# Kernel optimization log

Measured on AMD Instinct MI355X. Metric: run time of the kernel, lower is better.

## Reference

```python
import jax, jax.numpy as jnp
import numpy as np

N, D_IN, D_HID, D_OUT, E = 8192, 1024, 4096, 1024, 8
N_ACTIVE = max(1, int(E * 0.625))  # 5
TEMP = float(np.e)               # temperature = np.e in source


def setup_inputs() -> dict:
    key = jax.random.key(0)
    ks = jax.random.split(key, 4)
    return {
        "x": jax.random.normal(ks[0], (N, D_IN), jnp.float32),
        "gate_w": jax.random.normal(ks[1], (D_IN, E), jnp.float32) * 0.02,
        "gate_b": jnp.zeros((E,), jnp.float32),
        "w1": jax.random.normal(ks[2], (E, D_IN, D_HID), jnp.float32) * 0.02,
        "b1": jnp.zeros((E, D_HID), jnp.float32),
        "w2": jax.random.normal(ks[3], (E, D_HID, D_OUT), jnp.float32) * 0.02,
        "b2": jnp.zeros((E, D_OUT), jnp.float32),
    }


def reference(x, gate_w, gate_b, w1, b1, w2, b2):
    # Gate: softmax over experts at temperature e, then top-k mask + renormalize
    scores = (x @ gate_w + gate_b) / TEMP                 # [N, E]
    probs = jax.nn.softmax(scores, axis=-1)               # [N, E]
    _, topk_idx = jax.lax.top_k(probs, N_ACTIVE)          # [N, k]
    mask = jax.nn.one_hot(topk_idx, E, dtype=probs.dtype).sum(axis=-2)  # [N, E]
    weights = probs * mask
    weights = weights / (weights.sum(axis=-1, keepdims=True) + 1e-8)
    # Dense all-experts FFN (dropout is eval-mode identity)
    h = jax.nn.relu(jnp.einsum('nd,edh->neh', x, w1) + b1)   # [N, E, d_hid]
    e_out = jnp.einsum('neh,eho->neo', h, w2) + b2           # [N, E, d_out]
    # Camp A (first E/2 experts) added, camp G subtracted: out = out_a - out_g
    sign = jnp.where(jnp.arange(E) < E // 2, 1.0, -1.0)      # [E]
    return jnp.einsum('ne,neo->no', weights * sign, e_out)   # [N, d_out]
```

## Files before the change

kernel.cpp:

```cpp
#include <hip/hip_runtime.h>
#include <hip/hip_bf16.h>
#include <cmath>


typedef _Float16 f16;
typedef _Float16 f16x8 __attribute__((ext_vector_type(8)));
typedef _Float16 f16x4 __attribute__((ext_vector_type(4)));
typedef float f32x4 __attribute__((ext_vector_type(4)));

#define NROWS 8192
#define DIN   1024
#define DHID  4096
#define DOUT  1024
#define NEXP  8

#define OFF_SGATE 0u
#define OFF_XH    262144u
#define OFF_W1T   17039360u
#define OFF_W2T   84148224u
#define OFF_HHS   151257088u
#define OFF_PART  688128000u
#define NEED_PRIMARY 755236864ull
#define NEED_FALLBACK 218365952ull

__device__ __forceinline__ void gload_lds16(const void* gsrc, void* ldsdst) {
  __builtin_amdgcn_global_load_lds(
      (const __attribute__((address_space(1))) unsigned int*)gsrc,
      (__attribute__((address_space(3))) unsigned int*)ldsdst, 16, 0, 0);
}

__global__ void gate_kernel(const float* __restrict__ x,
                            const float* __restrict__ gw,
                            const float* __restrict__ gb,
                            float* __restrict__ sgate) {
  const int row = blockIdx.x * 4 + (threadIdx.x >> 6);
  const int l = threadIdx.x & 63;
  const float* xr = x + (size_t)row * DIN;
  float acc[8] = {0.f,0.f,0.f,0.f,0.f,0.f,0.f,0.f};
#pragma unroll
  for (int j = 0; j < 16; ++j) {
    const int k = l + 64 * j;
    const float xv = xr[k];
    const float4 g0 = *(const float4*)(gw + (size_t)k * 8);
    const float4 g1 = *(const float4*)(gw + (size_t)k * 8 + 4);
    acc[0] += xv * g0.x; acc[1] += xv * g0.y; acc[2] += xv * g0.z; acc[3] += xv * g0.w;
    acc[4] += xv * g1.x; acc[5] += xv * g1.y; acc[6] += xv * g1.z; acc[7] += xv * g1.w;
  }
#pragma unroll
  for (int off = 32; off > 0; off >>= 1) {
#pragma unroll
    for (int e = 0; e < 8; ++e) acc[e] += __shfl_xor(acc[e], off, 64);
  }
  if (l == 0) {
    const float invT = 0.36787944117144233f;
    float p[8]; float mx = -1e30f;
#pragma unroll
    for (int e = 0; e < 8; ++e) { p[e] = (acc[e] + gb[e]) * invT; mx = fmaxf(mx, p[e]); }
    float S = 0.f;
#pragma unroll
    for (int e = 0; e < 8; ++e) { p[e] = expf(p[e] - mx); S += p[e]; }
    const float inv = 1.0f / S;
#pragma unroll
    for (int e = 0; e < 8; ++e) p[e] *= inv;
    bool keep[8] = {true,true,true,true,true,true,true,true};
    for (int t = 0; t < 3; ++t) {
      float pmin = 1e30f; int mi = -1;
      for (int e = 0; e < 8; ++e)
        if (keep[e] && (p[e] < pmin || (p[e] == pmin && e > mi))) { pmin = p[e]; mi = e; }
      keep[mi] = false;
    }
    float wsum = 0.f;
#pragma unroll
    for (int e = 0; e < 8; ++e) if (keep[e]) wsum += p[e];
    const float rinv = 1.0f / (wsum + 1e-8f);
#pragma unroll
    for (int e = 0; e < 8; ++e) {
      const float wv = keep[e] ? p[e] * rinv : 0.0f;
      sgate[(size_t)row * 8 + e] = (e < 4) ? wv : -wv;
    }
  }
}

__global__ void cvt_x_kernel(const float* __restrict__ x, f16* __restrict__ xh) {
  const size_t i = ((size_t)blockIdx.x * blockDim.x + threadIdx.x) * 4;
  const float4 v = *(const float4*)(x + i);
  f16x4 o = { (f16)v.x, (f16)v.y, (f16)v.z, (f16)v.w };
  *(f16x4*)(xh + i) = o;
}

__global__ void transpose_cvt(const float* __restrict__ in, f16* __restrict__ out,
                              int R, int C) {
  __shared__ float tile[32][33];
  const int e = blockIdx.z;
  const float* ine = in + (size_t)e * R * C;
  f16* oute = out + (size_t)e * R * C;
  const int c0 = blockIdx.x * 32, r0 = blockIdx.y * 32;
  const int tx = threadIdx.x, ty = threadIdx.y;
#pragma unroll
  for (int i = 0; i < 4; ++i)
    tile[ty + i * 8][tx] = ine[(size_t)(r0 + ty + i * 8) * C + c0 + tx];
  __syncthreads();
#pragma unroll
  for (int i = 0; i < 4; ++i)
    oute[(size_t)(c0 + ty + i * 8) * R + r0 + tx] = (f16)tile[tx][ty + i * 8];
}

#define MFMAOP(a_, b_, c_) __builtin_amdgcn_mfma_f32_16x16x32_f16(a_, b_, c_, 0, 0, 0)

template <int EPI>
__global__ __launch_bounds__(512, 2) void gemm256(
    const f16* __restrict__ A, int lda,
    const f16* __restrict__ B, int ldb,
    const float* __restrict__ bias,
    f16* __restrict__ outH, int ldc,
    float* __restrict__ outP,
    const float* __restrict__ sgate, int expert, int gx) {
  __shared__ alignas(16) f16 lA[3 * 8192];
  __shared__ alignas(16) f16 lB[3 * 8192];
  const int tid = threadIdx.x;
  const int l = tid & 63, w = tid >> 6;
  const int wr = w >> 2, wc = w & 3;

  const int nwg = gridDim.x, cpx = nwg >> 3;
  const int lg = ((int)blockIdx.x & 7) * cpx + ((int)blockIdx.x >> 3);
  int m0, n0, kbase, nt;
  float* P = outP;
  const f16* Aeff = A;
  if constexpr (EPI == 1) {
    m0 = (lg / gx) * 256; n0 = (lg % gx) * 256; kbase = 0; nt = lda >> 5;
  } else {
    n0 = (lg & 3) * 256;
    const int kh = (lg >> 2) & 1;
    m0 = (lg >> 3) * 256;
    kbase = kh * 16384; nt = 512;
    Aeff = A + kbase;
    P = outP + (size_t)kh * 8388608;
  }

  const int rA = tid >> 2;
  const int cw = (tid & 3) ^ ((rA >> 1) & 3);
  const char* srcA1 = (const char*)(Aeff + (size_t)(m0 + rA) * lda + cw * 8);
  const char* srcA2 = srcA1 + (size_t)128 * lda * 2;
  const char* srcB1;
  const char* srcB2;
  if constexpr (EPI == 1) {
    srcB1 = (const char*)(B + (size_t)(n0 + rA) * ldb + cw * 8);
    srcB2 = srcB1 + (size_t)128 * ldb * 2;
  } else {
    srcB1 = (const char*)(B + (size_t)(n0 + rA) * 4096 + cw * 8);
    srcB2 = srcB1 + (size_t)128 * 4096 * 2;
  }

  int aoff[8], boff[4];
  {
    const int c = l >> 4;
#pragma unroll
    for (int f = 0; f < 8; ++f) {
      const int r = wr * 128 + f * 16 + (l & 15);
      aoff[f] = (r * 64 + ((c ^ ((r >> 1) & 3)) << 4)) >> 1;
    }
#pragma unroll
    for (int g = 0; g < 4; ++g) {
      const int r = wc * 64 + g * 16 + (l & 15);
      boff[g] = (r * 64 + ((c ^ ((r >> 1) & 3)) << 4)) >> 1;
    }
  }

  f32x4 acc[8][4] = {};
  f16x8 afr[8], bfr[4];

#define STAGE_A(dst, kb) do { \
    gload_lds16(srcA1 + (kb), (dst) + w * 512); \
    gload_lds16(srcA2 + (kb), (dst) + w * 512 + 4096); \
  } while (0)
#define STAGE_B(dst, kb) do { \
    gload_lds16(srcB1 + (kb), (dst) + w * 512); \
    gload_lds16(srcB2 + (kb), (dst) + w * 512 + 4096); \
  } while (0)
#define BAR() asm volatile("s_barrier" ::: "memory")
#define VM4() asm volatile("s_waitcnt vmcnt(4)" ::: "memory")
#define VM0() asm volatile("s_waitcnt vmcnt(0)" ::: "memory")

  auto akb = [&](int tk) -> size_t { return (size_t)tk * 64; };
  auto bkb = [&](int tk) -> size_t {
    if constexpr (EPI == 1) return (size_t)tk * 64;
    else {
      const int kg = kbase + tk * 32;
      return (size_t)(kg >> 12) * 8388608 + (size_t)(kg & 4095) * 2;
    }
  };

  f16 *cA = lA, *nA = lA + 8192, *sA = lA + 16384;
  f16 *cB = lB, *nB = lB + 8192, *sB = lB + 16384;

  STAGE_A(cA, akb(0)); STAGE_B(cB, bkb(0));
  STAGE_A(nA, akb(1)); STAGE_B(nB, bkb(1));
  VM4();
  BAR();

  for (int tk = 0; tk < nt; ++tk) {
#pragma unroll
    for (int g = 0; g < 4; ++g) bfr[g] = *(const f16x8*)(cB + boff[g]);
#pragma unroll
    for (int f = 0; f < 8; ++f) afr[f] = *(const f16x8*)(cA + aoff[f]);
    const int tk2 = tk + 2;
    if (tk2 < nt) {
      STAGE_A(sA, akb(tk2));
      STAGE_B(sB, bkb(tk2));
      VM4();
    } else if (tk + 1 < nt) {
      VM0();
    }
    BAR();
    __builtin_amdgcn_s_setprio(1);
#pragma unroll
    for (int f = 0; f < 8; ++f)
#pragma unroll
      for (int g = 0; g < 4; ++g)
        acc[f][g] = MFMAOP(afr[f], bfr[g], acc[f][g]);
    __builtin_amdgcn_s_setprio(0);
    BAR();
    f16* t;
    t = cA; cA = nA; nA = sA; sA = t;
    t = cB; cB = nB; nB = sB; sB = t;
  }
  VM0();

  if constexpr (EPI == 1) {
#pragma unroll
    for (int mi = 0; mi < 8; ++mi)
#pragma unroll
      for (int r = 0; r < 4; ++r) {
        const int row = m0 + wr * 128 + mi * 16 + (l >> 4) * 4 + r;
        const float sg = sgate[(size_t)row * 8 + expert];
#pragma unroll
        for (int ni = 0; ni < 4; ++ni) {
          const int col = n0 + wc * 64 + ni * 16 + (l & 15);
          const float v = acc[mi][ni][r] + bias[col];
          outH[(size_t)row * ldc + col] = (f16)(fmaxf(v, 0.0f) * sg);
        }
      }
  } else {
#pragma unroll
    for (int mi = 0; mi < 8; ++mi)
#pragma unroll
      for (int r = 0; r < 4; ++r) {
        const int row = m0 + wr * 128 + mi * 16 + (l >> 4) * 4 + r;
#pragma unroll
        for (int ni = 0; ni < 4; ++ni) {
          const int col = n0 + wc * 64 + ni * 16 + (l & 15);
          P[(size_t)row * 1024 + col] = acc[mi][ni][r];
        }
      }
  }
#undef STAGE_A
#undef STAGE_B
#undef BAR
#undef VM4
#undef VM0
}

template <bool WITHP>
__global__ void finalize_out(const float* __restrict__ p0,
                             const float* __restrict__ p1,
                             const float* __restrict__ sgate,
                             const float* __restrict__ b2,
                             float* __restrict__ out) {
  const int i = blockIdx.x * 256 + threadIdx.x;
  const int n = i >> 8, c4 = i & 255;
  float4 a = make_float4(0.f, 0.f, 0.f, 0.f);
  if constexpr (WITHP) {
    const float4 u = ((const float4*)p0)[i];
    const float4 v = ((const float4*)p1)[i];
    a.x = u.x + v.x; a.y = u.y + v.y; a.z = u.z + v.z; a.w = u.w + v.w;
  }
  const float* sg = sgate + (size_t)n * 8;
#pragma unroll
  for (int e = 0; e < 8; ++e) {
    const float s = sg[e];
    const float4 bv = ((const float4*)(b2 + (size_t)e * 1024))[c4];
    a.x += s * bv.x; a.y += s * bv.y; a.z += s * bv.z; a.w += s * bv.w;
  }
  ((float4*)out)[i] = a;
}

__global__ __launch_bounds__(512, 2) void gemm_acc(
    const f16* __restrict__ A, const f16* __restrict__ Bt,
    float* __restrict__ Out, int N, int K, int gx) {
  __shared__ alignas(16) f16 lA[3 * 256 * 64];
  __shared__ alignas(16) f16 lB[3 * 128 * 64];
  const int tid = threadIdx.x;
  const int l = tid & 63, w = tid >> 6;
  const int wr = w >> 1, wc = w & 1;
  const int nwg = gridDim.x, cpx = nwg >> 3;
  const int lg = ((int)blockIdx.x & 7) * cpx + ((int)blockIdx.x >> 3);
  const int bx = lg % gx, by = lg / gx;
  const int m0 = by * 256, n0 = bx * 128;

  const int srow = tid >> 3;
  const int scol = (((tid & 7) ^ (srow & 7)) << 3);
  const f16* Ab = A + ((size_t)m0 + srow) * K + scol;
  const f16* Bb = Bt + ((size_t)n0 + srow) * K + scol;
  f16* const dA = &lA[w * 512];
  f16* const dB = &lB[w * 512];

  int aoff[4][2], boff[4][2];
#pragma unroll
  for (int f = 0; f < 4; ++f) {
    const int ar = wr * 64 + f * 16 + (l & 15);
    const int br = wc * 64 + f * 16 + (l & 15);
#pragma unroll
    for (int ks = 0; ks < 2; ++ks) {
      const int cb = ks * 64 + ((l >> 4) << 4);
      aoff[f][ks] = ar * 64 + ((cb ^ ((ar & 7) << 4)) >> 1);
      boff[f][ks] = br * 64 + ((cb ^ ((br & 7) << 4)) >> 1);
    }
  }
  f32x4 acc[4][4] = {};
  f16x8 b[4][2];
  f16x8 aA, aB, aC, aD;
#define STAGE_A(bs, t) do { \
    const f16* s_ = Ab + (size_t)(t) * 64; \
    gload_lds16(s_,                   dA + (bs) * 16384); \
    gload_lds16(s_ + (size_t)64 * K,  dA + (bs) * 16384 + 4096); \
    gload_lds16(s_ + (size_t)128 * K, dA + (bs) * 16384 + 8192); \
    gload_lds16(s_ + (size_t)192 * K, dA + (bs) * 16384 + 12288); \
  } while (0)
#define STAGE_B(bs, t) do { \
    const f16* s_ = Bb + (size_t)(t) * 64; \
    gload_lds16(s_,                   dB + (bs) * 8192); \
    gload_lds16(s_ + (size_t)64 * K,  dB + (bs) * 8192 + 4096); \
  } while (0)
#define LOAD_B(bs) do { \
    b[0][0] = *(const f16x8*)&lB[(bs) * 8192 + boff[0][0]]; \
    b[0][1] = *(const f16x8*)&lB[(bs) * 8192 + boff[0][1]]; \
    b[1][0] = *(const f16x8*)&lB[(bs) * 8192 + boff[1][0]]; \
    b[1][1] = *(const f16x8*)&lB[(bs) * 8192 + boff[1][1]]; \
    b[2][0] = *(const f16x8*)&lB[(bs) * 8192 + boff[2][0]]; \
    b[2][1] = *(const f16x8*)&lB[(bs) * 8192 + boff[2][1]]; \
    b[3][0] = *(const f16x8*)&lB[(bs) * 8192 + boff[3][0]]; \
    b[3][1] = *(const f16x8*)&lB[(bs) * 8192 + boff[3][1]]; \
  } while (0)
#define LOAD_A4(bs, m0_, m1_) do { \
    aA = *(const f16x8*)&lA[(bs) * 16384 + aoff[m0_][0]]; \
    aB = *(const f16x8*)&lA[(bs) * 16384 + aoff[m0_][1]]; \
    aC = *(const f16x8*)&lA[(bs) * 16384 + aoff[m1_][0]]; \
    aD = *(const f16x8*)&lA[(bs) * 16384 + aoff[m1_][1]]; \
  } while (0)
#define CLUSTER(m0_, m1_) do { \
    __builtin_amdgcn_s_setprio(1); \
    acc[m0_][0] = MFMAOP(aA, b[0][0], acc[m0_][0]); \
    acc[m0_][1] = MFMAOP(aA, b[1][0], acc[m0_][1]); \
    acc[m0_][2] = MFMAOP(aA, b[2][0], acc[m0_][2]); \
    acc[m0_][3] = MFMAOP(aA, b[3][0], acc[m0_][3]); \
    acc[m1_][0] = MFMAOP(aC, b[0][0], acc[m1_][0]); \
    acc[m1_][1] = MFMAOP(aC, b[1][0], acc[m1_][1]); \
    acc[m1_][2] = MFMAOP(aC, b[2][0], acc[m1_][2]); \
    acc[m1_][3] = MFMAOP(aC, b[3][0], acc[m1_][3]); \
    acc[m0_][0] = MFMAOP(aB, b[0][1], acc[m0_][0]); \
    acc[m0_][1] = MFMAOP(aB, b[1][1], acc[m0_][1]); \
    acc[m0_][2] = MFMAOP(aB, b[2][1], acc[m0_][2]); \
    acc[m0_][3] = MFMAOP(aB, b[3][1], acc[m0_][3]); \
    acc[m1_][0] = MFMAOP(aD, b[0][1], acc[m1_][0]); \
    acc[m1_][1] = MFMAOP(aD, b[1][1], acc[m1_][1]); \
    acc[m1_][2] = MFMAOP(aD, b[2][1], acc[m1_][2]); \
    acc[m1_][3] = MFMAOP(aD, b[3][1], acc[m1_][3]); \
    __builtin_amdgcn_s_setprio(0); \
  } while (0)
#define BAR() asm volatile("s_barrier" ::: "memory")
#define VM6() asm volatile("s_waitcnt vmcnt(6)" ::: "memory")
  const int niter = K >> 7, ntiles = K >> 6;
  STAGE_A(0, 0); STAGE_B(0, 0);
  STAGE_A(1, 1); STAGE_B(1, 1);
  VM6();
  BAR();
  int bp = 0, bq = 1, brr = 2;
  int t2 = 2, t3 = 3;
  for (int i = 0; i < niter; ++i) {
    LOAD_B(bp); LOAD_A4(bp, 0, 1);
    STAGE_A(brr, t2);
    BAR(); CLUSTER(0, 1); BAR();
    LOAD_A4(bp, 2, 3);
    STAGE_B(brr, t2);
    VM6(); BAR(); CLUSTER(2, 3); BAR();
    LOAD_B(bq); LOAD_A4(bq, 0, 1);
    STAGE_A(bp, t3);
    BAR(); CLUSTER(0, 1); BAR();
    LOAD_A4(bq, 2, 3);
    STAGE_B(bp, t3);
    VM6(); BAR(); CLUSTER(2, 3); BAR();
    const int tmp = bp; bp = brr; brr = bq; bq = tmp;
    t2 += 2; if (t2 >= ntiles) t2 -= ntiles;
    t3 += 2; if (t3 >= ntiles) t3 -= ntiles;
  }
  asm volatile("s_waitcnt vmcnt(0)" ::: "memory");
#pragma unroll
  for (int mi = 0; mi < 4; ++mi)
#pragma unroll
    for (int r = 0; r < 4; ++r) {
      const int row = m0 + wr * 64 + mi * 16 + (l >> 4) * 4 + r;
#pragma unroll
      for (int ni = 0; ni < 4; ++ni) {
        const int col = n0 + wc * 64 + ni * 16 + (l & 15);
        Out[(size_t)row * N + col] += acc[mi][ni][r];
      }
    }
#undef STAGE_A
#undef STAGE_B
#undef LOAD_B
#undef LOAD_A4
#undef CLUSTER
#undef BAR
#undef VM6
}

extern "C" void kernel_launch(void* const* d_in, const int* in_sizes, int n_in,
                              void* d_out, int out_size, void* d_ws, size_t ws_size,
                              hipStream_t stream) {
  const float* x  = (const float*)d_in[0];
  const float* gw = (const float*)d_in[1];
  const float* gb = (const float*)d_in[2];
  const float* w1 = (const float*)d_in[3];
  const float* b1 = (const float*)d_in[4];
  const float* w2 = (const float*)d_in[5];
  const float* b2 = (const float*)d_in[6];
  float* out = (float*)d_out;

  char* ws = (char*)d_ws;
  float* sgate = (float*)(ws + OFF_SGATE);
  f16* xh  = (f16*)(ws + OFF_XH);
  f16* w1t = (f16*)(ws + OFF_W1T);
  f16* w2t = (f16*)(ws + OFF_W2T);
  f16* hhs = (f16*)(ws + OFF_HHS);
  float* part = (float*)(ws + OFF_PART);

  const bool primary = (ws_size >= NEED_PRIMARY);

  gate_kernel<<<NROWS / 4, 256, 0, stream>>>(x, gw, gb, sgate);
  cvt_x_kernel<<<(NROWS * DIN) / (256 * 4), 256, 0, stream>>>(x, xh);
  transpose_cvt<<<dim3(DHID / 32, DIN / 32, NEXP), dim3(32, 8), 0, stream>>>(w1, w1t, DIN, DHID);
  transpose_cvt<<<dim3(DOUT / 32, DHID / 32, NEXP), dim3(32, 8), 0, stream>>>(w2, w2t, DHID, DOUT);

  if (primary) {
    for (int e = 0; e < NEXP; ++e) {
      gemm256<1><<<512, 512, 0, stream>>>(
          xh, DIN, w1t + (size_t)e * DHID * DIN, DIN,
          b1 + (size_t)e * DHID, hhs + (size_t)e * DHID, NEXP * DHID,
          nullptr, sgate, e, DHID / 256);
    }
    gemm256<2><<<256, 512, 0, stream>>>(
        hhs, NEXP * DHID, w2t, DHID, nullptr, nullptr, 0, part, nullptr, 0, 0);
    finalize_out<true><<<(NROWS * DOUT) / (256 * 4), 256, 0, stream>>>(
        part, part + (size_t)NROWS * DOUT, sgate, b2, out);
  } else {
    finalize_out<false><<<(NROWS * DOUT) / (256 * 4), 256, 0, stream>>>(
        nullptr, nullptr, sgate, b2, out);
    for (int e = 0; e < NEXP; ++e) {
      gemm256<1><<<512, 512, 0, stream>>>(
          xh, DIN, w1t + (size_t)e * DHID * DIN, DIN,
          b1 + (size_t)e * DHID, hhs, DHID,
          nullptr, sgate, e, DHID / 256);
      gemm_acc<<<256, 512, 0, stream>>>(hhs, w2t + (size_t)e * DOUT * DHID,
                                        out, DOUT, DHID, DOUT / 128);
    }
  }
}
```

Before: 1.540 ms.

## Rewrite GEMM with 4-stage LDS pipeline, K=64 tiles, and per-expert split-K accumulation

The 256x256 GEMM is rewritten to use K=64 tiles with a 4-slot LDS ring, an XOR swizzle across 8 column groups, and four MFMA phases per tile that interleave fragment reads and async global-to-LDS staging. The primary path no longer builds one large hidden buffer for all experts followed by a single down-projection. Each expert now runs its up-projection, then a split-K down-projection that accumulates into the output and one partial buffer, which shrinks the workspace needed. The cost is more launches and read-modify-write traffic on the output for each expert, plus larger LDS use that may limit occupancy.

```diff
diff --git a/kernel.cpp b/kernel.cpp
--- a/kernel.cpp
+++ b/kernel.cpp
@@ -19,9 +19,8 @@
 #define OFF_W1T   17039360u
 #define OFF_W2T   84148224u
 #define OFF_HHS   151257088u
-#define OFF_PART  688128000u
-#define NEED_PRIMARY 755236864ull
-#define NEED_FALLBACK 218365952ull
+#define OFF_P1    218365952u
+#define NEED_MID  251920384ull
 
 __device__ __forceinline__ void gload_lds16(const void* gsrc, void* ldsdst) {
   __builtin_amdgcn_global_load_lds(
@@ -108,123 +107,139 @@
 #define MFMAOP(a_, b_, c_) __builtin_amdgcn_mfma_f32_16x16x32_f16(a_, b_, c_, 0, 0, 0)
 
 template <int EPI>
-__global__ __launch_bounds__(512, 2) void gemm256(
+__global__ __launch_bounds__(512, 2) void gemm8p(
     const f16* __restrict__ A, int lda,
-    const f16* __restrict__ B, int ldb,
+    const f16* __restrict__ B, int ldb, int nt,
     const float* __restrict__ bias,
     f16* __restrict__ outH, int ldc,
-    float* __restrict__ outP,
+    float* outP0, float* outP1, int p1w,
     const float* __restrict__ sgate, int expert, int gx) {
-  __shared__ alignas(16) f16 lA[3 * 8192];
-  __shared__ alignas(16) f16 lB[3 * 8192];
+  __shared__ alignas(16) f16 lA[4 * 8192];
+  __shared__ alignas(16) f16 lB[4 * 8192];
   const int tid = threadIdx.x;
   const int l = tid & 63, w = tid >> 6;
   const int wr = w >> 2, wc = w & 3;
 
   const int nwg = gridDim.x, cpx = nwg >> 3;
   const int lg = ((int)blockIdx.x & 7) * cpx + ((int)blockIdx.x >> 3);
-  int m0, n0, kbase, nt;
-  float* P = outP;
+
+  int m0, n0;
   const f16* Aeff = A;
+  const f16* Beff = B;
+  float* P = nullptr;
+  bool pw = false;
   if constexpr (EPI == 1) {
-    m0 = (lg / gx) * 256; n0 = (lg % gx) * 256; kbase = 0; nt = lda >> 5;
+    m0 = (lg / gx) * 256; n0 = (lg % gx) * 256;
   } else {
-    n0 = (lg & 3) * 256;
-    const int kh = (lg >> 2) & 1;
-    m0 = (lg >> 3) * 256;
-    kbase = kh * 16384; nt = 512;
-    Aeff = A + kbase;
-    P = outP + (size_t)kh * 8388608;
-  }
-
-  const int rA = tid >> 2;
-  const int cw = (tid & 3) ^ ((rA >> 1) & 3);
-  const char* srcA1 = (const char*)(Aeff + (size_t)(m0 + rA) * lda + cw * 8);
-  const char* srcA2 = srcA1 + (size_t)128 * lda * 2;
-  const char* srcB1;
-  const char* srcB2;
-  if constexpr (EPI == 1) {
-    srcB1 = (const char*)(B + (size_t)(n0 + rA) * ldb + cw * 8);
-    srcB2 = srcB1 + (size_t)128 * ldb * 2;
-  } else {
-    srcB1 = (const char*)(B + (size_t)(n0 + rA) * 4096 + cw * 8);
-    srcB2 = srcB1 + (size_t)128 * 4096 * 2;
-  }
-
-  int aoff[8], boff[4];
-  {
-    const int c = l >> 4;
-#pragma unroll
-    for (int f = 0; f < 8; ++f) {
-      const int r = wr * 128 + f * 16 + (l & 15);
-      aoff[f] = (r * 64 + ((c ^ ((r >> 1) & 3)) << 4)) >> 1;
-    }
-#pragma unroll
-    for (int g = 0; g < 4; ++g) {
-      const int r = wc * 64 + g * 16 + (l & 15);
-      boff[g] = (r * 64 + ((c ^ ((r >> 1) & 3)) << 4)) >> 1;
-    }
-  }
+    const int kh = lg & 1;
+    const int tt = lg >> 1;
+    m0 = (tt / gx) * 256; n0 = (tt % gx) * 256;
+    Aeff = A + kh * 2048;
+    Beff = B + kh * 2048;
+    P = kh ? outP1 : outP0;
+    pw = (p1w != 0);
+  }
+
+  const int srow = tid >> 3;
+  const int sxc = (tid & 7) ^ (srow & 7);
+  const f16* pA = Aeff + (size_t)(m0 + srow) * lda + sxc * 8;
+  const f16* pB = Beff + (size_t)(n0 + srow) * ldb + sxc * 8;
+  f16* const dA = lA + w * 512;
+  f16* const dB = lB + w * 512;
+
+#define STG_A(slot, h, tk) do { \
+    const f16* s_ = pA + (size_t)(h) * 128 * lda + (size_t)(tk) * 64; \
+    gload_lds16(s_,            dA + (slot) * 8192); \
+    gload_lds16(s_ + 64 * lda, dA + (slot) * 8192 + 4096); \
+  } while (0)
+#define STG_B(slot, h, tk) do { \
+    const f16* s_ = pB + (size_t)(h) * 128 * ldb + (size_t)(tk) * 64; \
+    gload_lds16(s_,            dB + (slot) * 8192); \
+    gload_lds16(s_ + 64 * ldb, dB + (slot) * 8192 + 4096); \
+  } while (0)
+
+  const int cg = l >> 4, xr = l & 7;
+  const int ok0 = ((cg ^ xr) << 4);
+  const int ok1 = (((4 + cg) ^ xr) << 4);
+  const char* const baA = (const char*)lA + (l & 15) * 128;
+  const char* const baB = (const char*)lB + (wc & 1) * 8192 + (l & 15) * 128;
+
+#define RDA(CA, f, o) (*(const f16x8*)(baA + ((CA) + wr) * 16384 + (f) * 2048 + (o)))
+#define RDB(CB, g, o) (*(const f16x8*)(baB + ((CB) + (wc >> 1)) * 16384 + (g) * 2048 + (o)))
+#define SYNC() do { __builtin_amdgcn_s_barrier(); \
+    asm volatile("s_waitcnt lgkmcnt(0)" ::: "memory"); \
+    __builtin_amdgcn_sched_barrier(0); } while (0)
+#define ENDPH() do { __builtin_amdgcn_s_setprio(0); \
+    __builtin_amdgcn_s_barrier(); } while (0)
+#define VM6() do { asm volatile("s_waitcnt vmcnt(6)" ::: "memory"); \
+    __builtin_amdgcn_sched_barrier(0); } while (0)
+#define MM(f, g, ar, br) acc[f][g] = MFMAOP(ar, br, acc[f][g])
 
   f32x4 acc[8][4] = {};
-  f16x8 afr[8], bfr[4];
-
-#define STAGE_A(dst, kb) do { \
-    gload_lds16(srcA1 + (kb), (dst) + w * 512); \
-    gload_lds16(srcA2 + (kb), (dst) + w * 512 + 4096); \
-  } while (0)
-#define STAGE_B(dst, kb) do { \
-    gload_lds16(srcB1 + (kb), (dst) + w * 512); \
-    gload_lds16(srcB2 + (kb), (dst) + w * 512 + 4096); \
-  } while (0)
-#define BAR() asm volatile("s_barrier" ::: "memory")
-#define VM4() asm volatile("s_waitcnt vmcnt(4)" ::: "memory")
-#define VM0() asm volatile("s_waitcnt vmcnt(0)" ::: "memory")
-
-  auto akb = [&](int tk) -> size_t { return (size_t)tk * 64; };
-  auto bkb = [&](int tk) -> size_t {
-    if constexpr (EPI == 1) return (size_t)tk * 64;
-    else {
-      const int kg = kbase + tk * 32;
-      return (size_t)(kg >> 12) * 8388608 + (size_t)(kg & 4095) * 2;
-    }
-  };
-
-  f16 *cA = lA, *nA = lA + 8192, *sA = lA + 16384;
-  f16 *cB = lB, *nB = lB + 8192, *sB = lB + 16384;
-
-  STAGE_A(cA, akb(0)); STAGE_B(cB, bkb(0));
-  STAGE_A(nA, akb(1)); STAGE_B(nB, bkb(1));
-  VM4();
-  BAR();
-
-  for (int tk = 0; tk < nt; ++tk) {
-#pragma unroll
-    for (int g = 0; g < 4; ++g) bfr[g] = *(const f16x8*)(cB + boff[g]);
-#pragma unroll
-    for (int f = 0; f < 8; ++f) afr[f] = *(const f16x8*)(cA + aoff[f]);
-    const int tk2 = tk + 2;
-    if (tk2 < nt) {
-      STAGE_A(sA, akb(tk2));
-      STAGE_B(sB, bkb(tk2));
-      VM4();
-    } else if (tk + 1 < nt) {
-      VM0();
-    }
-    BAR();
-    __builtin_amdgcn_s_setprio(1);
-#pragma unroll
-    for (int f = 0; f < 8; ++f)
-#pragma unroll
-      for (int g = 0; g < 4; ++g)
-        acc[f][g] = MFMAOP(afr[f], bfr[g], acc[f][g]);
-    __builtin_amdgcn_s_setprio(0);
-    BAR();
-    f16* t;
-    t = cA; cA = nA; nA = sA; sA = t;
-    t = cB; cB = nB; nB = sB; sB = t;
-  }
-  VM0();
+  f16x8 aA0,aA1,aB0,aB1,aC0,aC1,aD0,aD1;
+  f16x8 b00,b01,b10,b11,b20,b21,b30,b31;
+
+#define TILEBODY(T, CA, CB, SB1, SB0n, SA0n, SA1n) do { \
+     \
+    aA0 = RDA(CA, 0, ok0); aA1 = RDA(CA, 0, ok1); \
+    aB0 = RDA(CA, 1, ok0); aB1 = RDA(CA, 1, ok1); \
+    aC0 = RDA(CA, 2, ok0); aC1 = RDA(CA, 2, ok1); \
+    aD0 = RDA(CA, 3, ok0); aD1 = RDA(CA, 3, ok1); \
+    b00 = RDB(CB, 0, ok0); b01 = RDB(CB, 0, ok1); \
+    b10 = RDB(CB, 1, ok0); b11 = RDB(CB, 1, ok1); \
+    if ((T) + 1 < nt) STG_B(SB1, 1, (T) + 1); \
+    SYNC(); \
+    __builtin_amdgcn_s_setprio(1); \
+    MM(0,0,aA0,b00); MM(0,1,aA0,b10); MM(1,0,aB0,b00); MM(1,1,aB0,b10); \
+    MM(2,0,aC0,b00); MM(2,1,aC0,b10); MM(3,0,aD0,b00); MM(3,1,aD0,b10); \
+    MM(0,0,aA1,b01); MM(0,1,aA1,b11); MM(1,0,aB1,b01); MM(1,1,aB1,b11); \
+    MM(2,0,aC1,b01); MM(2,1,aC1,b11); MM(3,0,aD1,b01); MM(3,1,aD1,b11); \
+    ENDPH(); \
+     \
+    b20 = RDB(CB, 2, ok0); b21 = RDB(CB, 2, ok1); \
+    b30 = RDB(CB, 3, ok0); b31 = RDB(CB, 3, ok1); \
+    SYNC(); \
+    __builtin_amdgcn_s_setprio(1); \
+    MM(0,2,aA0,b20); MM(0,3,aA0,b30); MM(1,2,aB0,b20); MM(1,3,aB0,b30); \
+    MM(2,2,aC0,b20); MM(2,3,aC0,b30); MM(3,2,aD0,b20); MM(3,3,aD0,b30); \
+    MM(0,2,aA1,b21); MM(0,3,aA1,b31); MM(1,2,aB1,b21); MM(1,3,aB1,b31); \
+    MM(2,2,aC1,b21); MM(2,3,aC1,b31); MM(3,2,aD1,b21); MM(3,3,aD1,b31); \
+    ENDPH(); \
+     \
+    aA0 = RDA(CA, 4, ok0); aA1 = RDA(CA, 4, ok1); \
+    aB0 = RDA(CA, 5, ok0); aB1 = RDA(CA, 5, ok1); \
+    aC0 = RDA(CA, 6, ok0); aC1 = RDA(CA, 6, ok1); \
+    aD0 = RDA(CA, 7, ok0); aD1 = RDA(CA, 7, ok1); \
+    if ((T) + 2 < nt) STG_B(SB0n, 0, (T) + 2); \
+    SYNC(); \
+    __builtin_amdgcn_s_setprio(1); \
+    MM(4,0,aA0,b00); MM(4,1,aA0,b10); MM(5,0,aB0,b00); MM(5,1,aB0,b10); \
+    MM(6,0,aC0,b00); MM(6,1,aC0,b10); MM(7,0,aD0,b00); MM(7,1,aD0,b10); \
+    MM(4,0,aA1,b01); MM(4,1,aA1,b11); MM(5,0,aB1,b01); MM(5,1,aB1,b11); \
+    MM(6,0,aC1,b01); MM(6,1,aC1,b11); MM(7,0,aD1,b01); MM(7,1,aD1,b11); \
+    ENDPH(); \
+     \
+    if ((T) + 2 < nt) { STG_A(SA0n, 0, (T) + 2); STG_A(SA1n, 1, (T) + 2); } \
+    VM6(); \
+    SYNC(); \
+    __builtin_amdgcn_s_setprio(1); \
+    MM(4,2,aA0,b20); MM(4,3,aA0,b30); MM(5,2,aB0,b20); MM(5,3,aB0,b30); \
+    MM(6,2,aC0,b20); MM(6,3,aC0,b30); MM(7,2,aD0,b20); MM(7,3,aD0,b30); \
+    MM(4,2,aA1,b21); MM(4,3,aA1,b31); MM(5,2,aB1,b21); MM(5,3,aB1,b31); \
+    MM(6,2,aC1,b21); MM(6,3,aC1,b31); MM(7,2,aD1,b21); MM(7,3,aD1,b31); \
+    ENDPH(); \
+  } while (0)
+
+  STG_A(0, 0, 0); STG_B(0, 0, 0); STG_A(1, 1, 0); STG_B(1, 1, 0);
+  STG_A(2, 0, 1); STG_B(2, 0, 1); STG_A(3, 1, 1);
+  asm volatile("s_waitcnt vmcnt(6)" ::: "memory");
+  __builtin_amdgcn_s_barrier();
+
+  for (int t = 0; t < nt; t += 2) {
+    TILEBODY(t,     0, 0, 3, 0, 0, 1);
+    TILEBODY(t + 1, 2, 2, 1, 2, 2, 3);
+  }
+  asm volatile("s_waitcnt vmcnt(0)" ::: "memory");
 
   if constexpr (EPI == 1) {
 #pragma unroll
@@ -249,23 +264,30 @@
 #pragma unroll
         for (int ni = 0; ni < 4; ++ni) {
           const int col = n0 + wc * 64 + ni * 16 + (l & 15);
-          P[(size_t)row * 1024 + col] = acc[mi][ni][r];
+          const size_t ix = (size_t)row * 1024 + col;
+          float v = acc[mi][ni][r];
+          if (!pw) v += P[ix];
+          P[ix] = v;
         }
       }
   }
-#undef STAGE_A
-#undef STAGE_B
-#undef BAR
-#undef VM4
-#undef VM0
+#undef STG_A
+#undef STG_B
+#undef RDA
+#undef RDB
+#undef SYNC
+#undef ENDPH
+#undef VM6
+#undef MM
+#undef TILEBODY
 }
 
 template <bool WITHP>
-__global__ void finalize_out(const float* __restrict__ p0,
+__global__ void finalize_out(const float* p0,
                              const float* __restrict__ p1,
                              const float* __restrict__ sgate,
                              const float* __restrict__ b2,
-                             float* __restrict__ out) {
+                             float* out) {
   const int i = blockIdx.x * 256 + threadIdx.x;
   const int n = i >> 8, c4 = i & 255;
   float4 a = make_float4(0.f, 0.f, 0.f, 0.f);
@@ -368,11 +390,11 @@
     __builtin_amdgcn_s_setprio(0); \
   } while (0)
 #define BAR() asm volatile("s_barrier" ::: "memory")
-#define VM6() asm volatile("s_waitcnt vmcnt(6)" ::: "memory")
+#define VMC6() asm volatile("s_waitcnt vmcnt(6)" ::: "memory")
   const int niter = K >> 7, ntiles = K >> 6;
   STAGE_A(0, 0); STAGE_B(0, 0);
   STAGE_A(1, 1); STAGE_B(1, 1);
-  VM6();
+  VMC6();
   BAR();
   int bp = 0, bq = 1, brr = 2;
   int t2 = 2, t3 = 3;
@@ -382,13 +404,13 @@
     BAR(); CLUSTER(0, 1); BAR();
     LOAD_A4(bp, 2, 3);
     STAGE_B(brr, t2);
-    VM6(); BAR(); CLUSTER(2, 3); BAR();
+    VMC6(); BAR(); CLUSTER(2, 3); BAR();
     LOAD_B(bq); LOAD_A4(bq, 0, 1);
     STAGE_A(bp, t3);
     BAR(); CLUSTER(0, 1); BAR();
     LOAD_A4(bq, 2, 3);
     STAGE_B(bp, t3);
-    VM6(); BAR(); CLUSTER(2, 3); BAR();
+    VMC6(); BAR(); CLUSTER(2, 3); BAR();
     const int tmp = bp; bp = brr; brr = bq; bq = tmp;
     t2 += 2; if (t2 >= ntiles) t2 -= ntiles;
     t3 += 2; if (t3 >= ntiles) t3 -= ntiles;
@@ -411,7 +433,7 @@
 #undef LOAD_A4
 #undef CLUSTER
 #undef BAR
-#undef VM6
+#undef VMC6
 }
 
 extern "C" void kernel_launch(void* const* d_in, const int* in_sizes, int n_in,
@@ -432,34 +454,35 @@
   f16* w1t = (f16*)(ws + OFF_W1T);
   f16* w2t = (f16*)(ws + OFF_W2T);
   f16* hhs = (f16*)(ws + OFF_HHS);
-  float* part = (float*)(ws + OFF_PART);
-
-  const bool primary = (ws_size >= NEED_PRIMARY);
+  float* p1 = (float*)(ws + OFF_P1);
+
+  const bool mid = (ws_size >= NEED_MID);
 
   gate_kernel<<<NROWS / 4, 256, 0, stream>>>(x, gw, gb, sgate);
   cvt_x_kernel<<<(NROWS * DIN) / (256 * 4), 256, 0, stream>>>(x, xh);
   transpose_cvt<<<dim3(DHID / 32, DIN / 32, NEXP), dim3(32, 8), 0, stream>>>(w1, w1t, DIN, DHID);
   transpose_cvt<<<dim3(DOUT / 32, DHID / 32, NEXP), dim3(32, 8), 0, stream>>>(w2, w2t, DHID, DOUT);
 
-  if (primary) {
+  if (mid) {
     for (int e = 0; e < NEXP; ++e) {
-      gemm256<1><<<512, 512, 0, stream>>>(
-          xh, DIN, w1t + (size_t)e * DHID * DIN, DIN,
-          b1 + (size_t)e * DHID, hhs + (size_t)e * DHID, NEXP * DHID,
-          nullptr, sgate, e, DHID / 256);
-    }
-    gemm256<2><<<256, 512, 0, stream>>>(
-        hhs, NEXP * DHID, w2t, DHID, nullptr, nullptr, 0, part, nullptr, 0, 0);
+      gemm8p<1><<<512, 512, 0, stream>>>(
+          xh, DIN, w1t + (size_t)e * DHID * DIN, DIN, DIN / 64,
+          b1 + (size_t)e * DHID, hhs, DHID,
+          nullptr, nullptr, 0, sgate, e, DHID / 256);
+      gemm8p<2><<<256, 512, 0, stream>>>(
+          hhs, DHID, w2t + (size_t)e * DOUT * DHID, DHID, 2048 / 64,
+          nullptr, nullptr, 0, out, p1, (e == 0) ? 1 : 0, nullptr, 0, DOUT / 256);
+    }
     finalize_out<true><<<(NROWS * DOUT) / (256 * 4), 256, 0, stream>>>(
-        part, part + (size_t)NROWS * DOUT, sgate, b2, out);
+        out, p1, sgate, b2, out);
   } else {
     finalize_out<false><<<(NROWS * DOUT) / (256 * 4), 256, 0, stream>>>(
         nullptr, nullptr, sgate, b2, out);
     for (int e = 0; e < NEXP; ++e) {
-      gemm256<1><<<512, 512, 0, stream>>>(
-          xh, DIN, w1t + (size_t)e * DHID * DIN, DIN,
+      gemm8p<1><<<512, 512, 0, stream>>>(
+          xh, DIN, w1t + (size_t)e * DHID * DIN, DIN, DIN / 64,
           b1 + (size_t)e * DHID, hhs, DHID,
-          nullptr, sgate, e, DHID / 256);
+          nullptr, nullptr, 0, sgate, e, DHID / 256);
       gemm_acc<<<256, 512, 0, stream>>>(hhs, w2t + (size_t)e * DOUT * DHID,
                                         out, DOUT, DHID, DOUT / 128);
     }
```

After: 1.504 ms. -2.3%, faster.
